# Performance work log

Hardware: AMD Instinct MI355X
Metric: run time of the kernel (lower is better)

## Reference

```python
import jax, jax.numpy as jnp
import numpy as np

N_NODES = 40000
N_EDGES = 480000
MULT = 64
NUM_SPECIES = 5
N_BASIS = 8
MLP_HIDDEN = 64
AVG_NEIGH = 12.0

INV8 = float(1.0 / np.sqrt(8.0))
INV64 = float(1.0 / np.sqrt(64.0))
INV128 = float(1.0 / np.sqrt(128.0))


def _poly_envelope(x):
    # e3nn.poly_envelope(5, 2) == DimeNet-style cutoff with p=6:
    # f(0)=1, first 5 derivatives zero at 0, f and 2 derivatives zero at 1.
    u = 1.0 - 28.0 * x**6 + 48.0 * x**7 - 21.0 * x**8
    return jnp.where(x < 1.0, u, 0.0)


def setup_inputs() -> dict:
    key = jax.random.key(0)
    ks = jax.random.split(key, 15)
    vectors = jax.random.uniform(ks[0], (N_EDGES, 3), jnp.float32, -0.5, 0.5)
    node_scalars = jax.random.normal(ks[1], (N_NODES, MULT), jnp.float32)
    node_vectors = jax.random.normal(ks[2], (N_NODES, MULT, 3), jnp.float32)
    node_specie = jax.random.randint(ks[3], (N_NODES,), 0, NUM_SPECIES)
    senders = jax.random.randint(ks[4], (N_EDGES,), 0, N_NODES)
    receivers = jax.random.randint(ks[5], (N_EDGES,), 0, N_NODES)
    # learned params (e3nn Linear weights ~ N(0,1), fwd divides by sqrt(fan_in))
    W_up_s = jax.random.normal(ks[6], (MULT, MULT), jnp.float32)
    W_up_v = jax.random.normal(ks[7], (MULT, MULT), jnp.float32)
    W_skip_s = jax.random.normal(ks[8], (NUM_SPECIES, MULT, 2 * MULT), jnp.float32)
    W_skip_v = jax.random.normal(ks[9], (NUM_SPECIES, MULT, MULT), jnp.float32)
    W_mlp1 = jax.random.normal(ks[10], (N_BASIS, MLP_HIDDEN), jnp.float32)
    W_mlp2 = jax.random.normal(ks[11], (MLP_HIDDEN, MLP_HIDDEN), jnp.float32)
    W_mlp3 = jax.random.normal(ks[12], (MLP_HIDDEN, 4 * MULT), jnp.float32)
    W_down_s = jax.random.normal(ks[13], (2 * MULT, 2 * MULT), jnp.float32)
    W_down_v = jax.random.normal(ks[14], (2 * MULT, MULT), jnp.float32)
    return dict(vectors=vectors, node_scalars=node_scalars, node_vectors=node_vectors,
                node_specie=node_specie, senders=senders, receivers=receivers,
                W_up_s=W_up_s, W_up_v=W_up_v, W_skip_s=W_skip_s, W_skip_v=W_skip_v,
                W_mlp1=W_mlp1, W_mlp2=W_mlp2, W_mlp3=W_mlp3,
                W_down_s=W_down_s, W_down_v=W_down_v)


def reference(vectors, node_scalars, node_vectors, node_specie, senders, receivers,
              W_up_s, W_up_v, W_skip_s, W_skip_v, W_mlp1, W_mlp2, W_mlp3,
              W_down_s, W_down_v):
    N = node_scalars.shape[0]
    # self-connection: species-indexed linear ('skip_tp'), output 128x0e + 64x1o
    sc_s = jnp.einsum('ni,nio->no', node_scalars, W_skip_s[node_specie]) * INV64
    sc_v = jnp.einsum('nic,nio->noc', node_vectors, W_skip_v[node_specie]) * INV64
    # linear_up (irreps-wise linear, 64x0e+64x1o -> same)
    h_s = (node_scalars @ W_up_s) * INV64
    h_v = jnp.einsum('nic,io->noc', node_vectors, W_up_v) * INV64
    # gather by sender
    m_s = h_s[senders]                       # [E,64]
    m_v = h_v[senders]                       # [E,64,3]
    # spherical harmonics l=1, normalize=True, component norm: sqrt(3)*r_hat
    lengths = jnp.linalg.norm(vectors, axis=1, keepdims=True)   # [E,1]
    safe_len = jnp.where(lengths == 0.0, 1.0, lengths)
    Y = jnp.sqrt(3.0) * vectors / safe_len                      # [E,3]
    # sparse CG tensor product (component norm): 0e x 1o -> 1o, 1o x 1o -> 0e
    tp_1o = m_s[:, :, None] * Y[:, None, :]                     # [E,64,3]
    tp_0e = jnp.einsum('eic,ec->ei', m_v, Y) / jnp.sqrt(3.0)    # [E,64]
    # concatenate + regroup -> 128x0e + 128x1o
    msg_s = jnp.concatenate([m_s, tp_0e], axis=1)               # [E,128]
    msg_v = jnp.concatenate([m_v, tp_1o], axis=1)               # [E,128,3]
    # radial basis (bessel, x_max=1) * smooth envelope
    k = jnp.arange(1, N_BASIS + 1, dtype=jnp.float32)
    bes = jnp.sqrt(2.0) * jnp.sin(k * jnp.pi * safe_len) / safe_len  # [E,8]
    rb = jnp.where(lengths == 0.0, 0.0, bes * _poly_envelope(lengths))
    h = jax.nn.swish((rb @ W_mlp1) * INV8)
    h = jax.nn.swish((h @ W_mlp2) * INV64)
    mix = (h @ W_mlp3) * INV64                                  # [E,256]
    msg_s = msg_s * mix[:, :128]
    msg_v = msg_v * mix[:, 128:, None]
    # scatter-add to receivers, normalize by sqrt(avg_num_neighbors)
    inv_sqrt_nn = 1.0 / np.sqrt(AVG_NEIGH)
    agg_s = jax.ops.segment_sum(msg_s, receivers, num_segments=N) * inv_sqrt_nn
    agg_v = jax.ops.segment_sum(msg_v, receivers, num_segments=N) * inv_sqrt_nn
    # linear_down to 128x0e + 64x1o, plus self-connection
    d_s = (agg_s @ W_down_s) * INV128 + sc_s                    # [N,128]
    d_v = jnp.einsum('nic,io->noc', agg_v, W_down_v) * INV128 + sc_v  # [N,64,3]
    # gate: first 64 scalars kept (swish), last 64 gate the vectors (swish)
    out_s = jax.nn.swish(d_s[:, :MULT])
    gates = jax.nn.swish(d_s[:, MULT:])
    out_v = d_v * gates[:, :, None]
    return jnp.concatenate([out_s, out_v.reshape(N, MULT * 3)], axis=1)  # [N,256]
```

## Files before the change

kernel.cpp:

```cpp
#include <hip/hip_runtime.h>
#include <hip/hip_bf16.h>

#define N_NODES 40000
#define N_EDGES 480000
#define SEG 2
#define SEG_E (N_EDGES / SEG)
#define SEG_TILES (SEG_E / 16)
#define SCAN_BLOCKS 157

typedef short bf16x8 __attribute__((ext_vector_type(8)));
typedef float f32x4 __attribute__((ext_vector_type(4)));

__device__ __forceinline__ float bf2f(__hip_bfloat16 x) { return __bfloat162float(x); }

__device__ __forceinline__ float swishf(float x) { return x / (1.0f + __expf(-x)); }

__device__ __forceinline__ float bflo(unsigned u) { union { unsigned u; float f; } w; w.u = u << 16; return w.f; }
__device__ __forceinline__ float bfhi(unsigned u) { union { unsigned u; float f; } w; w.u = u & 0xffff0000u; return w.f; }
__device__ __forceinline__ float bfu(unsigned short u) { union { unsigned u; float f; } w; w.u = ((unsigned)u) << 16; return w.f; }

__device__ __forceinline__ unsigned short f2bf_bits(float x) {
    union { __hip_bfloat16 h; unsigned short u; } c; c.h = __float2bfloat16(x); return c.u;
}

__constant__ const float INV8 = 0.35355339059327373f;
__constant__ const float INV64 = 0.125f;
__constant__ const float INV128 = 0.08838834764831845f;
__constant__ const float INV_NN = 0.2886751345948129f;
__constant__ const float SQRT2 = 1.4142135623730951f;
__constant__ const float SQRT3 = 1.7320508075688772f;
__constant__ const float INV_SQRT3 = 0.5773502691896258f;
__constant__ const float PI_F = 3.14159265358979323846f;

__device__ __forceinline__ float LDf(const void* p, size_t i, bool f32) {
    float v;
    if (f32) v = ((const float*)p)[i];
    else     v = bf2f(((const __hip_bfloat16*)p)[i]);
    return v;
}
__device__ __forceinline__ void load_f8r(const void* p, size_t i, bool f32, float* out) {
    if (f32) {
        const float4* q4 = (const float4*)((const float*)p + i);
        float4 a = q4[0], b = q4[1];
        out[0] = a.x; out[1] = a.y; out[2] = a.z; out[3] = a.w;
        out[4] = b.x; out[5] = b.y; out[6] = b.z; out[7] = b.w;
    } else {
        bf16x8 v = *(const bf16x8*)((const unsigned short*)p + i);
        #pragma unroll
        for (int j = 0; j < 8; j++) out[j] = bfu((unsigned short)v[j]);
    }
}

__global__ void detect_kernel(const unsigned short* __restrict__ w, int* __restrict__ flag) {
    int lane = threadIdx.x;
    int cnt = 0;
    for (int i = lane; i < 2048; i += 64) {
        unsigned e = (w[2 * i] >> 7) & 0xFF;
        if (e >= 110 && e <= 133) cnt++;
    }
    #pragma unroll
    for (int off = 32; off > 0; off >>= 1) cnt += __shfl_down(cnt, off, 64);
    if (lane == 0) *flag = (cnt > 1024) ? 1 : 0;
}

__global__ __launch_bounds__(256) void wprep_kernel(
    const void* __restrict__ W_up_s, const void* __restrict__ W_up_v,
    const void* __restrict__ W_skip_s, const void* __restrict__ W_skip_v,
    const void* __restrict__ W_down_s, const void* __restrict__ W_down_v,
    const void* __restrict__ W_mlp2, const void* __restrict__ W_mlp3,
    unsigned short* __restrict__ Wup_sq, unsigned short* __restrict__ Wup_vq,
    unsigned short* __restrict__ Wq_s, unsigned short* __restrict__ Wq_v,
    unsigned short* __restrict__ W2q, unsigned short* __restrict__ W3q,
    const int* __restrict__ flag)
{
    bool f32 = (*flag == 0);
    const float SC = INV128 * INV_NN;
    int gid = blockIdx.x * 256 + threadIdx.x;
    int gs = gridDim.x * 256;
    for (int i = gid; i < 4096; i += gs) {
        int o = i & 63, k = i >> 6;
        Wup_sq[o * 72 + k] = f2bf_bits(LDf(W_up_s, k * 64 + o, f32) * INV64);
        Wup_vq[o * 72 + k] = f2bf_bits(LDf(W_up_v, k * 64 + o, f32) * INV64);
    }
    for (int i = gid; i < 5 * 128 * 192; i += gs) {
        int sp = i / 24576, r = i - sp * 24576;
        int o = r / 192, k = r - o * 192;
        float w = (k < 128) ? LDf(W_down_s, k * 128 + o, f32) * SC
                            : LDf(W_skip_s, sp * 8192 + (k - 128) * 128 + o, f32) * INV64;
        Wq_s[sp * 25600 + o * 200 + k] = f2bf_bits(w);
    }
    for (int i = gid; i < 5 * 64 * 192; i += gs) {
        int sp = i / 12288, r = i - sp * 12288;
        int o = r / 192, k = r - o * 192;
        float w = (k < 128) ? LDf(W_down_v, k * 64 + o, f32) * SC
                            : LDf(W_skip_v, sp * 4096 + (k - 128) * 64 + o, f32) * INV64;
        Wq_v[sp * 12800 + o * 200 + k] = f2bf_bits(w);
    }
    for (int i = gid; i < 16384; i += gs) {
        int o = i & 255, k = i >> 8;
        W3q[o * 72 + k] = f2bf_bits(LDf(W_mlp3, k * 256 + o, f32));
    }
    for (int i = gid; i < 4096; i += gs) {
        int o = i & 63, k = i >> 6;
        W2q[o * 72 + k] = f2bf_bits(LDf(W_mlp2, k * 64 + o, f32));
    }
}

__global__ __launch_bounds__(256) void hist_kernel(const int* __restrict__ receivers,
                                                   int* __restrict__ cnt) {
    int e = blockIdx.x * 256 + threadIdx.x;
    if (e < N_EDGES) atomicAdd(&cnt[receivers[e]], 1);
}

__global__ __launch_bounds__(256) void partial_kernel(const int* __restrict__ cnt,
                                                      int* __restrict__ partials) {
    __shared__ int red[4];
    int idx = blockIdx.x * 256 + threadIdx.x;
    int v = (idx < N_NODES) ? cnt[idx] : 0;
    #pragma unroll
    for (int off = 32; off > 0; off >>= 1) v += __shfl_down(v, off, 64);
    int wave = threadIdx.x >> 6, lane = threadIdx.x & 63;
    if (lane == 0) red[wave] = v;
    __syncthreads();
    if (threadIdx.x == 0) partials[blockIdx.x] = red[0] + red[1] + red[2] + red[3];
}

__global__ __launch_bounds__(256) void scanp_kernel(const int* __restrict__ partials,
                                                    int* __restrict__ pscan) {
    __shared__ int buf[256];
    int t = threadIdx.x;
    int v = (t < SCAN_BLOCKS) ? partials[t] : 0;
    buf[t] = v;
    __syncthreads();
    for (int off = 1; off < 256; off <<= 1) {
        int tmp = (t >= off) ? buf[t - off] : 0;
        __syncthreads();
        buf[t] += tmp;
        __syncthreads();
    }
    if (t < SCAN_BLOCKS) pscan[t] = buf[t] - v;
}

__global__ __launch_bounds__(256) void offs_kernel(const int* __restrict__ cnt,
                                                   const int* __restrict__ pscan,
                                                   int* __restrict__ offs,
                                                   int* __restrict__ cursor) {
    __shared__ int buf[256];
    int b = blockIdx.x, t = threadIdx.x;
    int idx = b * 256 + t;
    int v = (idx < N_NODES) ? cnt[idx] : 0;
    buf[t] = v;
    __syncthreads();
    for (int off = 1; off < 256; off <<= 1) {
        int tmp = (t >= off) ? buf[t - off] : 0;
        __syncthreads();
        buf[t] += tmp;
        __syncthreads();
    }
    int exc = buf[t] - v + pscan[b];
    if (idx < N_NODES) { offs[idx] = exc; cursor[idx] = exc; }
    if (idx == N_NODES - 1) offs[N_NODES] = exc + v;
}

__global__ __launch_bounds__(256) void scatter_kernel(const int* __restrict__ receivers,
                                                      const int* __restrict__ senders,
                                                      int* __restrict__ cursor,
                                                      int* __restrict__ sorted_eid,
                                                      int* __restrict__ sorted_snd) {
    int e = blockIdx.x * 256 + threadIdx.x;
    if (e < N_EDGES) {
        int p = atomicAdd(&cursor[receivers[e]], 1);
        sorted_eid[p] = e;
        sorted_snd[p] = senders[e];
    }
}

__global__ __launch_bounds__(256) void hist5_kernel(const int* __restrict__ specie,
                                                    int* __restrict__ cnt5) {
    int n = blockIdx.x * 256 + threadIdx.x;
    int lane = threadIdx.x & 63;
    int sp = (n < N_NODES) ? specie[n] : -1;
    #pragma unroll
    for (int s = 0; s < 5; s++) {
        unsigned long long mask = __ballot(sp == s);
        if (mask != 0ull) {
            int leader = __builtin_ctzll(mask);
            if (lane == leader) atomicAdd(&cnt5[s], __popcll(mask));
        }
    }
}

__global__ void scan5_kernel(const int* __restrict__ cnt5, int* __restrict__ sp_offs,
                             int* __restrict__ cursor5, int* __restrict__ tile_info) {
    if (threadIdx.x != 0 || blockIdx.x != 0) return;
    int run = 0, tb = 0;
    for (int s = 0; s < 5; s++) {
        sp_offs[s] = run; cursor5[s] = run;
        tile_info[s] = tb;
        int c = cnt5[s];
        int T = (c + 15) >> 4;
        tile_info[8 + s] = T;
        tb += (T + 3) >> 2;
        run += c;
    }
    sp_offs[5] = run;
    tile_info[5] = tb;
}

__global__ __launch_bounds__(256) void scatter5_kernel(const int* __restrict__ specie,
                                                       int* __restrict__ cursor5,
                                                       int* __restrict__ sorted_node) {
    int n = blockIdx.x * 256 + threadIdx.x;
    int lane = threadIdx.x & 63;
    int sp = (n < N_NODES) ? specie[n] : -1;
    #pragma unroll
    for (int s = 0; s < 5; s++) {
        unsigned long long mask = __ballot(sp == s);
        if (mask != 0ull) {
            int leader = __builtin_ctzll(mask);
            int base = 0;
            if (lane == leader) base = atomicAdd(&cursor5[s], __popcll(mask));
            base = __shfl(base, leader);
            if (sp == s) {
                int prefix = __popcll(mask & ((1ull << lane) - 1ull));
                sorted_node[base + prefix] = n;
            }
        }
    }
}

__global__ __launch_bounds__(256) void node_up_kernel(
    const void* __restrict__ node_scalars,
    const void* __restrict__ node_vectors,
    const unsigned short* __restrict__ Wup_sq,
    const unsigned short* __restrict__ Wup_vq,
    unsigned short* __restrict__ hbuf,
    unsigned short* __restrict__ ns_b,
    unsigned short* __restrict__ nv_t,
    const int* __restrict__ flag)
{
    bool f32 = (*flag == 0);
    __shared__ __align__(16) unsigned short WsT[64 * 72];
    __shared__ __align__(16) unsigned short WvT[64 * 72];
    int tid = threadIdx.x;
    for (int i = tid; i < 576; i += 256) {
        ((uint4*)WsT)[i] = ((const uint4*)Wup_sq)[i];
        ((uint4*)WvT)[i] = ((const uint4*)Wup_vq)[i];
    }
    __syncthreads();
    int wave = tid >> 6, lane = tid & 63;
    int m = lane & 15, q = lane >> 4;
    int base = (blockIdx.x * 4 + wave) * 16;

    f32x4 accS[4];
    f32x4 accV[3][4];
    #pragma unroll
    for (int t = 0; t < 4; t++) {
        accS[t] = f32x4{0.f, 0.f, 0.f, 0.f};
        #pragma unroll
        for (int c = 0; c < 3; c++) accV[c][t] = f32x4{0.f, 0.f, 0.f, 0.f};
    }

    #pragma unroll
    for (int kk = 0; kk < 2; kk++) {
        int i0 = kk * 32 + 8 * q;
        float fs[8];
        load_f8r(node_scalars, (size_t)(base + m) * 64 + i0, f32, fs);
        bf16x8 aS;
        #pragma unroll
        for (int j = 0; j < 8; j++) aS[j] = (short)f2bf_bits(fs[j]);
        *(bf16x8*)(ns_b + (size_t)(base + m) * 64 + i0) = aS;
        float fv[24];
        size_t vbase = (size_t)(base + m) * 192 + (size_t)i0 * 3;
        load_f8r(node_vectors, vbase,      f32, fv);
        load_f8r(node_vectors, vbase + 8,  f32, fv + 8);
        load_f8r(node_vectors, vbase + 16, f32, fv + 16);
        bf16x8 aV[3];
        #pragma unroll
        for (int c = 0; c < 3; c++) {
            #pragma unroll
            for (int j = 0; j < 8; j++) aV[c][j] = (short)f2bf_bits(fv[3 * j + c]);
            *(bf16x8*)(nv_t + (size_t)c * N_NODES * 64 + (size_t)(base + m) * 64 + i0) = aV[c];
        }
        #pragma unroll
        for (int t = 0; t < 4; t++) {
            bf16x8 bS = *(const bf16x8*)(WsT + (16 * t + m) * 72 + kk * 32 + 8 * q);
            bf16x8 bV = *(const bf16x8*)(WvT + (16 * t + m) * 72 + kk * 32 + 8 * q);
            accS[t]    = __builtin_amdgcn_mfma_f32_16x16x32_bf16(aS,    bS, accS[t],    0, 0, 0);
            accV[0][t] = __builtin_amdgcn_mfma_f32_16x16x32_bf16(aV[0], bV, accV[0][t], 0, 0, 0);
            accV[1][t] = __builtin_amdgcn_mfma_f32_16x16x32_bf16(aV[1], bV, accV[1][t], 0, 0, 0);
            accV[2][t] = __builtin_amdgcn_mfma_f32_16x16x32_bf16(aV[2], bV, accV[2][t], 0, 0, 0);
        }
    }
    #pragma unroll
    for (int t = 0; t < 4; t++) {
        #pragma unroll
        for (int r = 0; r < 4; r++) {
            uint2 pk;
            pk.x = (unsigned)f2bf_bits(accS[t][r])    | ((unsigned)f2bf_bits(accV[0][t][r]) << 16);
            pk.y = (unsigned)f2bf_bits(accV[1][t][r]) | ((unsigned)f2bf_bits(accV[2][t][r]) << 16);
            *(uint2*)(hbuf + (size_t)(base + 4 * q + r) * 256 + (16 * t + m) * 4) = pk;
        }
    }
}

__global__ __launch_bounds__(512) void mlp_kernel(
    const void* __restrict__ vectors,
    const int* __restrict__ sorted_eid,
    const void* __restrict__ W1,
    const unsigned short* __restrict__ W2q,
    const unsigned short* __restrict__ W3q,
    unsigned short* __restrict__ mixseg,
    unsigned short* __restrict__ yq,
    int p_lo,
    const int* __restrict__ flag)
{
    bool f32 = (*flag == 0);
    __shared__ __align__(16) unsigned short W3T[256 * 72];
    __shared__ __align__(16) unsigned short W2T[64 * 72];
    __shared__ unsigned short hbl[8 * 64 * 17];
    int tid = threadIdx.x;
    for (int i = tid; i < 2304; i += 512) ((uint4*)W3T)[i] = ((const uint4*)W3q)[i];
    for (int i = tid; i < 576; i += 512)  ((uint4*)W2T)[i] = ((const uint4*)W2q)[i];
    __syncthreads();
    int wave = tid >> 6, lane = tid & 63;
    int m = lane & 15, q = lane >> 4;
    int tile = blockIdx.x * 8 + wave;
    if (tile >= SEG_TILES) return;
    int p = p_lo + tile * 16 + m;

    int e = sorted_eid[p];
    float vx = LDf(vectors, (size_t)e * 3 + 0, f32);
    float vy = LDf(vectors, (size_t)e * 3 + 1, f32);
    float vz = LDf(vectors, (size_t)e * 3 + 2, f32);
    float len2 = vx * vx + vy * vy + vz * vz;
    float len = sqrtf(len2);
    float Yx = 0.f, Yy = 0.f, Yz = 0.f;
    float rb[8];
    if (len > 0.f) {
        float inv = 1.f / len;
        Yx = SQRT3 * vx * inv; Yy = SQRT3 * vy * inv; Yz = SQRT3 * vz * inv;
        float x6 = len2 * len2 * len2;
        float env = (len < 1.f) ? fmaf(x6, fmaf(len, fmaf(len, -21.f, 48.f), -28.f), 1.f) : 0.f;
        float c = SQRT2 * inv * env;
        #pragma unroll
        for (int k = 0; k < 8; k++) rb[k] = c * __sinf((float)(k + 1) * PI_F * len);
    } else {
        #pragma unroll
        for (int k = 0; k < 8; k++) rb[k] = 0.f;
    }
    if (q == 0) {
        uint2 yw;
        yw.x = f2bf_bits(Yx) | ((unsigned)f2bf_bits(Yy) << 16);
        yw.y = f2bf_bits(Yz);
        *(uint2*)(yq + (size_t)p * 4) = yw;
    }

    f32x4 zero4 = {0.f, 0.f, 0.f, 0.f};
    unsigned short* hb = hbl + wave * (64 * 17);

    bf16x8 b_rb;
    #pragma unroll
    for (int j = 0; j < 8; j++) b_rb[j] = (q == 0) ? (short)f2bf_bits(rb[j]) : (short)0;
    #pragma unroll
    for (int t = 0; t < 4; t++) {
        bf16x8 a;
        #pragma unroll
        for (int j = 0; j < 8; j++) a[j] = 0;
        if (q == 0) {
            #pragma unroll
            for (int j = 0; j < 8; j++)
                a[j] = (short)f2bf_bits(LDf(W1, j * 64 + 16 * t + m, f32));
        }
        f32x4 c = __builtin_amdgcn_mfma_f32_16x16x32_bf16(a, b_rb, zero4, 0, 0, 0);
        #pragma unroll
        for (int r = 0; r < 4; r++)
            hb[(16 * t + 4 * q + r) * 17 + m] = f2bf_bits(swishf(c[r] * INV8));
    }
    bf16x8 b2[2];
    #pragma unroll
    for (int h = 0; h < 2; h++)
        #pragma unroll
        for (int j = 0; j < 8; j++)
            b2[h][j] = (short)hb[(32 * h + 8 * q + j) * 17 + m];
    #pragma unroll
    for (int t = 0; t < 4; t++) {
        bf16x8 a0 = *(const bf16x8*)(W2T + (16 * t + m) * 72 + 8 * q);
        bf16x8 a1 = *(const bf16x8*)(W2T + (16 * t + m) * 72 + 32 + 8 * q);
        f32x4 c = __builtin_amdgcn_mfma_f32_16x16x32_bf16(a0, b2[0], zero4, 0, 0, 0);
        c = __builtin_amdgcn_mfma_f32_16x16x32_bf16(a1, b2[1], c, 0, 0, 0);
        #pragma unroll
        for (int r = 0; r < 4; r++)
            hb[(16 * t + 4 * q + r) * 17 + m] = f2bf_bits(swishf(c[r] * INV64));
    }
    bf16x8 b3[2];
    #pragma unroll
    for (int h = 0; h < 2; h++)
        #pragma unroll
        for (int j = 0; j < 8; j++)
            b3[h][j] = (short)hb[(32 * h + 8 * q + j) * 17 + m];
    size_t rowbase = ((size_t)(tile * 16 + m)) * 256;
    #pragma unroll
    for (int t3 = 0; t3 < 16; t3++) {
        bf16x8 a0 = *(const bf16x8*)(W3T + (16 * t3 + m) * 72 + 8 * q);
        bf16x8 a1 = *(const bf16x8*)(W3T + (16 * t3 + m) * 72 + 32 + 8 * q);
        f32x4 c = __builtin_amdgcn_mfma_f32_16x16x32_bf16(a0, b3[0], zero4, 0, 0, 0);
        c = __builtin_amdgcn_mfma_f32_16x16x32_bf16(a1, b3[1], c, 0, 0, 0);
        uint2 v;
        v.x = f2bf_bits(c[0] * INV64) | ((unsigned)f2bf_bits(c[1] * INV64) << 16);
        v.y = f2bf_bits(c[2] * INV64) | ((unsigned)f2bf_bits(c[3] * INV64) << 16);
        *(uint2*)(mixseg + rowbase + 16 * t3 + 4 * q) = v;
    }
}

__global__ __launch_bounds__(256) void agg_kernel(
    const unsigned short* __restrict__ hbuf,
    const int* __restrict__ sorted_snd,
    const unsigned short* __restrict__ mixseg,
    const unsigned short* __restrict__ yq,
    const int* __restrict__ offs,
    unsigned short* __restrict__ agg_s_b,
    unsigned short* __restrict__ agg_v_b,
    int slo, int shi)
{
    int tid = threadIdx.x, wave = tid >> 6, lane = tid & 63;
    int n = blockIdx.x * 4 + wave;
    if (n >= N_NODES) return;
    int beg = __builtin_amdgcn_readfirstlane(offs[n]);
    int end = __builtin_amdgcn_readfirstlane(offs[n + 1]);
    int lo = beg > slo ? beg : slo;
    int hi = end < shi ? end : shi;
    bool owner = (beg >= slo && beg < shi) || (beg >= shi && shi == N_EDGES);
    if (!owner && hi <= lo) return;
    unsigned short* aS = agg_s_b + (size_t)n * 128;
    unsigned short* aV = agg_v_b + (size_t)n * 384;
    float s0, s1, v0, v1, v2, v3, v4, v5;
    if (owner) {
        s0 = s1 = v0 = v1 = v2 = v3 = v4 = v5 = 0.f;
    } else {
        s0 = bfu(aS[lane]); s1 = bfu(aS[64 + lane]);
        v0 = bfu(aV[lane]); v1 = bfu(aV[64 + lane]); v2 = bfu(aV[128 + lane]);
        v3 = bfu(aV[192 + lane]); v4 = bfu(aV[256 + lane]); v5 = bfu(aV[320 + lane]);
    }
    for (int chunk = lo; chunk < hi; chunk += 64) {
        int cc = hi - chunk; if (cc > 64) cc = 64;
        int sv = (lane < cc) ? sorted_snd[chunk + lane] : 0;
        int i = 0;
        for (; i + 1 < cc; i += 2) {
            int snd0 = __builtin_amdgcn_readlane(sv, i);
            int snd1 = __builtin_amdgcn_readlane(sv, i + 1);
            int p0 = chunk + i, p1 = chunk + i + 1;
            uint2 h0 = *(const uint2*)(hbuf + (size_t)snd0 * 256 + lane * 4);
            uint2 h1 = *(const uint2*)(hbuf + (size_t)snd1 * 256 + lane * 4);
            const unsigned short* mp0 = mixseg + (size_t)(p0 - slo) * 256;
            const unsigned short* mp1 = mixseg + (size_t)(p1 - slo) * 256;
            float a0 = bfu(mp0[lane]), a1 = bfu(mp0[64 + lane]);
            float a2 = bfu(mp0[128 + lane]), a3 = bfu(mp0[192 + lane]);
            float b0 = bfu(mp1[lane]), b1 = bfu(mp1[64 + lane]);
            float b2 = bfu(mp1[128 + lane]), b3 = bfu(mp1[192 + lane]);
            uint2 yw0 = *(const uint2*)(yq + (size_t)p0 * 4);
            uint2 yw1 = *(const uint2*)(yq + (size_t)p1 * 4);
            {
                float m_s = bflo(h0.x), mv0 = bfhi(h0.x), mv1 = bflo(h0.y), mv2 = bfhi(h0.y);
                float Yx = bflo(yw0.x), Yy = bfhi(yw0.x), Yz = bflo(yw0.y);
                float tp0 = (mv0 * Yx + mv1 * Yy + mv2 * Yz) * INV_SQRT3;
                s0 = fmaf(m_s, a0, s0);
                s1 = fmaf(tp0, a1, s1);
                float t1 = m_s * a3;
                v0 = fmaf(mv0, a2, v0); v1 = fmaf(t1, Yx, v1);
                v2 = fmaf(mv1, a2, v2); v3 = fmaf(t1, Yy, v3);
                v4 = fmaf(mv2, a2, v4); v5 = fmaf(t1, Yz, v5);
            }
            {
                float m_s = bflo(h1.x), mv0 = bfhi(h1.x), mv1 = bflo(h1.y), mv2 = bfhi(h1.y);
                float Yx = bflo(yw1.x), Yy = bfhi(yw1.x), Yz = bflo(yw1.y);
                float tp0 = (mv0 * Yx + mv1 * Yy + mv2 * Yz) * INV_SQRT3;
                s0 = fmaf(m_s, b0, s0);
                s1 = fmaf(tp0, b1, s1);
                float t1 = m_s * b3;
                v0 = fmaf(mv0, b2, v0); v1 = fmaf(t1, Yx, v1);
                v2 = fmaf(mv1, b2, v2); v3 = fmaf(t1, Yy, v3);
                v4 = fmaf(mv2, b2, v4); v5 = fmaf(t1, Yz, v5);
            }
        }
        if (i < cc) {
            int snd = __builtin_amdgcn_readlane(sv, i);
            int p = chunk + i;
            uint2 hbv = *(const uint2*)(hbuf + (size_t)snd * 256 + lane * 4);
            const unsigned short* mp = mixseg + (size_t)(p - slo) * 256;
            float mix0 = bfu(mp[lane]), mix1 = bfu(mp[64 + lane]);
            float mix2 = bfu(mp[128 + lane]), mix3 = bfu(mp[192 + lane]);
            uint2 yw = *(const uint2*)(yq + (size_t)p * 4);
            float m_s = bflo(hbv.x), mv0 = bfhi(hbv.x), mv1 = bflo(hbv.y), mv2 = bfhi(hbv.y);
            float Yx = bflo(yw.x), Yy = bfhi(yw.x), Yz = bflo(yw.y);
            float tp0 = (mv0 * Yx + mv1 * Yy + mv2 * Yz) * INV_SQRT3;
            s0 = fmaf(m_s, mix0, s0);
            s1 = fmaf(tp0, mix1, s1);
            float t1 = m_s * mix3;
            v0 = fmaf(mv0, mix2, v0); v1 = fmaf(t1, Yx, v1);
            v2 = fmaf(mv1, mix2, v2); v3 = fmaf(t1, Yy, v3);
            v4 = fmaf(mv2, mix2, v4); v5 = fmaf(t1, Yz, v5);
        }
    }
    aS[lane] = f2bf_bits(s0); aS[64 + lane] = f2bf_bits(s1);
    aV[lane] = f2bf_bits(v0); aV[64 + lane] = f2bf_bits(v1); aV[128 + lane] = f2bf_bits(v2);
    aV[192 + lane] = f2bf_bits(v3); aV[256 + lane] = f2bf_bits(v4); aV[320 + lane] = f2bf_bits(v5);
}

__global__ __launch_bounds__(256) void node_final_kernel(
    const unsigned short* __restrict__ Wq_s,
    const unsigned short* __restrict__ Wq_v,
    const unsigned short* __restrict__ ns_b,
    const unsigned short* __restrict__ nv_t,
    const unsigned short* __restrict__ agg_s_b,
    const unsigned short* __restrict__ agg_v_b,
    const int* __restrict__ sorted_node,
    const int* __restrict__ sp_offs,
    const int* __restrict__ tile_info,
    void* __restrict__ out,
    const int* __restrict__ flag)
{
    bool f32 = (*flag == 0);
    int b = blockIdx.x;
    if (b >= tile_info[5]) return;
    __shared__ __align__(16) unsigned short As[128 * 200];
    __shared__ __align__(16) unsigned short Av[64 * 200];
    int sp = 0;
    #pragma unroll
    for (int s = 1; s < 5; s++) if (b >= tile_info[s]) sp = s;
    int tid = threadIdx.x;
    const uint4* ps = (const uint4*)(Wq_s + (size_t)sp * 25600);
    for (int i = tid; i < 3200; i += 256) ((uint4*)As)[i] = ps[i];
    const uint4* pv = (const uint4*)(Wq_v + (size_t)sp * 12800);
    for (int i = tid; i < 1600; i += 256) ((uint4*)Av)[i] = pv[i];
    __syncthreads();
    int wave = tid >> 6, lane = tid & 63;
    int m = lane & 15, q = lane >> 4;
    int T = tile_info[8 + sp];
    int tl = (b - tile_info[sp]) * 4 + wave;
    if (tl >= T) return;
    int row = sp_offs[sp] + tl * 16;
    int cnt = sp_offs[sp + 1] - row; if (cnt > 16) cnt = 16;
    int mm = (m < cnt) ? m : 0;
    int node = sorted_node[row + mm];

    bf16x8 bs[6];
    {
        const unsigned short* a = agg_s_b + (size_t)node * 128;
        #pragma unroll
        for (int f = 0; f < 4; f++) bs[f] = *(const bf16x8*)(a + f * 32 + q * 8);
        const unsigned short* s = ns_b + (size_t)node * 64;
        #pragma unroll
        for (int f = 0; f < 2; f++) bs[4 + f] = *(const bf16x8*)(s + f * 32 + q * 8);
    }
    bf16x8 bv[3][6];
    #pragma unroll
    for (int c = 0; c < 3; c++) {
        const unsigned short* a = agg_v_b + (size_t)node * 384 + c * 128;
        #pragma unroll
        for (int f = 0; f < 4; f++) bv[c][f] = *(const bf16x8*)(a + f * 32 + q * 8);
        const unsigned short* s = nv_t + (size_t)c * N_NODES * 64 + (size_t)node * 64;
        #pragma unroll
        for (int f = 0; f < 2; f++) bv[c][4 + f] = *(const bf16x8*)(s + f * 32 + q * 8);
    }
    f32x4 z4 = {0.f, 0.f, 0.f, 0.f};
    float gate[4][4];
    #pragma unroll
    for (int t = 0; t < 4; t++) {
        f32x4 c = z4;
        #pragma unroll
        for (int f = 0; f < 6; f++) {
            bf16x8 a = *(const bf16x8*)(As + (16 * (4 + t) + m) * 200 + f * 32 + q * 8);
            c = __builtin_amdgcn_mfma_f32_16x16x32_bf16(a, bs[f], c, 0, 0, 0);
        }
        #pragma unroll
        for (int r = 0; r < 4; r++) gate[t][r] = swishf(c[r]);
    }
    #pragma unroll
    for (int t = 0; t < 4; t++) {
        f32x4 c = z4;
        #pragma unroll
        for (int f = 0; f < 6; f++) {
            bf16x8 a = *(const bf16x8*)(As + (16 * t + m) * 200 + f * 32 + q * 8);
            c = __builtin_amdgcn_mfma_f32_16x16x32_bf16(a, bs[f], c, 0, 0, 0);
        }
        if (m < cnt) {
            size_t base = (size_t)node * 256 + 16 * t + 4 * q;
            if (f32) {
                float4 o4 = { swishf(c[0]), swishf(c[1]), swishf(c[2]), swishf(c[3]) };
                *(float4*)((float*)out + base) = o4;
            } else {
                uint2 o2;
                o2.x = f2bf_bits(swishf(c[0])) | ((unsigned)f2bf_bits(swishf(c[1])) << 16);
                o2.y = f2bf_bits(swishf(c[2])) | ((unsigned)f2bf_bits(swishf(c[3])) << 16);
                *(uint2*)((unsigned short*)out + base) = o2;
            }
        }
    }
    #pragma unroll
    for (int t = 0; t < 4; t++) {
        f32x4 c0 = z4, c1 = z4, c2 = z4;
        #pragma unroll
        for (int f = 0; f < 6; f++) {
            bf16x8 a = *(const bf16x8*)(Av + (16 * t + m) * 200 + f * 32 + q * 8);
            c0 = __builtin_amdgcn_mfma_f32_16x16x32_bf16(a, bv[0][f], c0, 0, 0, 0);
            c1 = __builtin_amdgcn_mfma_f32_16x16x32_bf16(a, bv[1][f], c1, 0, 0, 0);
            c2 = __builtin_amdgcn_mfma_f32_16x16x32_bf16(a, bv[2][f], c2, 0, 0, 0);
        }
        if (m < cnt) {
            #pragma unroll
            for (int r = 0; r < 4; r++) {
                float g = gate[t][r];
                int o = 16 * t + 4 * q + r;
                size_t base = (size_t)node * 256 + 64 + (size_t)o * 3;
                if (f32) {
                    ((float*)out)[base + 0] = c0[r] * g;
                    ((float*)out)[base + 1] = c1[r] * g;
                    ((float*)out)[base + 2] = c2[r] * g;
                } else {
                    ((__hip_bfloat16*)out)[base + 0] = __float2bfloat16(c0[r] * g);
                    ((__hip_bfloat16*)out)[base + 1] = __float2bfloat16(c1[r] * g);
                    ((__hip_bfloat16*)out)[base + 2] = __float2bfloat16(c2[r] * g);
                }
            }
        }
    }
}

extern "C" void kernel_launch(void* const* d_in, const int* in_sizes, int n_in,
                              void* d_out, int out_size, void* d_ws, size_t ws_size,
                              hipStream_t stream) {
    const void* vectors      = d_in[0];
    const void* node_scalars = d_in[1];
    const void* node_vectors = d_in[2];
    const int* node_specie   = (const int*)d_in[3];
    const int* senders       = (const int*)d_in[4];
    const int* receivers     = (const int*)d_in[5];
    const void* W_up_s       = d_in[6];
    const void* W_up_v       = d_in[7];
    const void* W_skip_s     = d_in[8];
    const void* W_skip_v     = d_in[9];
    const void* W_mlp1       = d_in[10];
    const void* W_mlp2       = d_in[11];
    const void* W_mlp3       = d_in[12];
    const void* W_down_s     = d_in[13];
    const void* W_down_v     = d_in[14];

    char* ws = (char*)d_ws;
    size_t off = 0;
    auto alloc = [&](size_t bytes) { void* p = ws + off; off += (bytes + 255) & ~(size_t)255; return p; };
    unsigned short* hbuf     = (unsigned short*)alloc((size_t)N_NODES * 256 * 2);
    unsigned short* ns_b     = (unsigned short*)alloc((size_t)N_NODES * 64 * 2);
    unsigned short* nv_t     = (unsigned short*)alloc((size_t)N_NODES * 192 * 2);
    unsigned short* agg_s_b  = (unsigned short*)alloc((size_t)N_NODES * 128 * 2);
    unsigned short* agg_v_b  = (unsigned short*)alloc((size_t)N_NODES * 384 * 2);
    unsigned short* mixseg   = (unsigned short*)alloc((size_t)SEG_E * 256 * 2);
    unsigned short* yq       = (unsigned short*)alloc((size_t)N_EDGES * 4 * 2);
    unsigned short* Wup_sq   = (unsigned short*)alloc((size_t)64 * 72 * 2);
    unsigned short* Wup_vq   = (unsigned short*)alloc((size_t)64 * 72 * 2);
    unsigned short* Wq_s     = (unsigned short*)alloc((size_t)5 * 128 * 200 * 2);
    unsigned short* Wq_v     = (unsigned short*)alloc((size_t)5 * 64 * 200 * 2);
    unsigned short* W2q      = (unsigned short*)alloc((size_t)64 * 72 * 2);
    unsigned short* W3q      = (unsigned short*)alloc((size_t)256 * 72 * 2);
    int* cnt        = (int*)alloc((size_t)(N_NODES + 8) * 4);
    int* cnt5       = cnt + N_NODES;
    int* offs       = (int*)alloc((size_t)(N_NODES + 1) * 4);
    int* cursor     = (int*)alloc((size_t)N_NODES * 4);
    int* sorted     = (int*)alloc((size_t)N_EDGES * 4);
    int* sorted_snd = (int*)alloc((size_t)N_EDGES * 4);
    int* sorted_node= (int*)alloc((size_t)N_NODES * 4);
    int* sp_offs    = (int*)alloc(16 * 4);
    int* cursor5    = (int*)alloc(16 * 4);
    int* tile_info  = (int*)alloc(16 * 4);
    int* partials   = (int*)alloc((size_t)(SCAN_BLOCKS + 1) * 4);
    int* pscan      = (int*)alloc((size_t)(SCAN_BLOCKS + 1) * 4);
    int* flag       = (int*)alloc(4);

    detect_kernel<<<dim3(1), dim3(64), 0, stream>>>((const unsigned short*)W_up_s, flag);
    hipMemsetAsync(cnt, 0, (size_t)(N_NODES + 8) * 4, stream);

    wprep_kernel<<<dim3(64), dim3(256), 0, stream>>>(
        W_up_s, W_up_v, W_skip_s, W_skip_v, W_down_s, W_down_v, W_mlp2, W_mlp3,
        Wup_sq, Wup_vq, Wq_s, Wq_v, W2q, W3q, flag);

    hist_kernel<<<dim3(1875), dim3(256), 0, stream>>>(receivers, cnt);
    partial_kernel<<<dim3(SCAN_BLOCKS), dim3(256), 0, stream>>>(cnt, partials);
    scanp_kernel<<<dim3(1), dim3(256), 0, stream>>>(partials, pscan);
    offs_kernel<<<dim3(SCAN_BLOCKS), dim3(256), 0, stream>>>(cnt, pscan, offs, cursor);
    scatter_kernel<<<dim3(1875), dim3(256), 0, stream>>>(receivers, senders, cursor, sorted, sorted_snd);

    hist5_kernel<<<dim3(157), dim3(256), 0, stream>>>(node_specie, cnt5);
    scan5_kernel<<<dim3(1), dim3(64), 0, stream>>>(cnt5, sp_offs, cursor5, tile_info);
    scatter5_kernel<<<dim3(157), dim3(256), 0, stream>>>(node_specie, cursor5, sorted_node);

    node_up_kernel<<<dim3(625), dim3(256), 0, stream>>>(
        node_scalars, node_vectors, Wup_sq, Wup_vq, hbuf, ns_b, nv_t, flag);

    const int MLP_BLOCKS = (SEG_TILES + 7) / 8;
    for (int s = 0; s < SEG; s++) {
        int p_lo = s * SEG_E;
        mlp_kernel<<<dim3(MLP_BLOCKS), dim3(512), 0, stream>>>(
            vectors, sorted, W_mlp1, W2q, W3q, mixseg, yq, p_lo, flag);
        agg_kernel<<<dim3(10000), dim3(256), 0, stream>>>(
            hbuf, sorted_snd, mixseg, yq, offs, agg_s_b, agg_v_b, p_lo, p_lo + SEG_E);
    }

    node_final_kernel<<<dim3(640), dim3(256), 0, stream>>>(
        Wq_s, Wq_v, ns_b, nv_t, agg_s_b, agg_v_b,
        sorted_node, sp_offs, tile_info, d_out, flag);
}
```

Measured before the change: 544.1 us.

## Pre-sort edge vectors in scatter and process multiple tiles per wave in MLP

The scatter kernel now writes each edge's vector as a float4 into receiver-sorted order, so the MLP kernel reads vectors contiguously instead of gathering through an edge-id indirection. The MLP kernel loops over four tiles per wave, which amortizes the per-block LDS staging of W2/W3 and the W1 fragment loads over more work. The LDS row padding for the hidden buffer changes from 17 to 18. The costs are an extra 16-byte-per-edge buffer and fewer blocks, which reduces parallelism and latency hiding in the MLP launch.

```diff
diff --git a/kernel.cpp b/kernel.cpp
--- a/kernel.cpp
+++ b/kernel.cpp
@@ -7,6 +7,7 @@
 #define SEG_E (N_EDGES / SEG)
 #define SEG_TILES (SEG_E / 16)
 #define SCAN_BLOCKS 157
+#define TPW 4
 
 typedef short bf16x8 __attribute__((ext_vector_type(8)));
 typedef float f32x4 __attribute__((ext_vector_type(4)));
@@ -164,14 +165,20 @@
 
 __global__ __launch_bounds__(256) void scatter_kernel(const int* __restrict__ receivers,
                                                       const int* __restrict__ senders,
+                                                      const void* __restrict__ vectors,
                                                       int* __restrict__ cursor,
-                                                      int* __restrict__ sorted_eid,
-                                                      int* __restrict__ sorted_snd) {
+                                                      int* __restrict__ sorted_snd,
+                                                      float4* __restrict__ sorted_vec,
+                                                      const int* __restrict__ flag) {
+    bool f32 = (*flag == 0);
     int e = blockIdx.x * 256 + threadIdx.x;
     if (e < N_EDGES) {
+        float vx = LDf(vectors, (size_t)e * 3 + 0, f32);
+        float vy = LDf(vectors, (size_t)e * 3 + 1, f32);
+        float vz = LDf(vectors, (size_t)e * 3 + 2, f32);
         int p = atomicAdd(&cursor[receivers[e]], 1);
-        sorted_eid[p] = e;
         sorted_snd[p] = senders[e];
+        sorted_vec[p] = float4{vx, vy, vz, 0.f};
     }
 }
 
@@ -305,8 +312,7 @@
 }
 
 __global__ __launch_bounds__(512) void mlp_kernel(
-    const void* __restrict__ vectors,
-    const int* __restrict__ sorted_eid,
+    const float4* __restrict__ sorted_vec,
     const void* __restrict__ W1,
     const unsigned short* __restrict__ W2q,
     const unsigned short* __restrict__ W3q,
@@ -318,98 +324,104 @@
     bool f32 = (*flag == 0);
     __shared__ __align__(16) unsigned short W3T[256 * 72];
     __shared__ __align__(16) unsigned short W2T[64 * 72];
-    __shared__ unsigned short hbl[8 * 64 * 17];
+    __shared__ unsigned short hbl[8 * 64 * 18];
     int tid = threadIdx.x;
     for (int i = tid; i < 2304; i += 512) ((uint4*)W3T)[i] = ((const uint4*)W3q)[i];
     for (int i = tid; i < 576; i += 512)  ((uint4*)W2T)[i] = ((const uint4*)W2q)[i];
     __syncthreads();
     int wave = tid >> 6, lane = tid & 63;
     int m = lane & 15, q = lane >> 4;
-    int tile = blockIdx.x * 8 + wave;
-    if (tile >= SEG_TILES) return;
-    int p = p_lo + tile * 16 + m;
-
-    int e = sorted_eid[p];
-    float vx = LDf(vectors, (size_t)e * 3 + 0, f32);
-    float vy = LDf(vectors, (size_t)e * 3 + 1, f32);
-    float vz = LDf(vectors, (size_t)e * 3 + 2, f32);
-    float len2 = vx * vx + vy * vy + vz * vz;
-    float len = sqrtf(len2);
-    float Yx = 0.f, Yy = 0.f, Yz = 0.f;
-    float rb[8];
-    if (len > 0.f) {
-        float inv = 1.f / len;
-        Yx = SQRT3 * vx * inv; Yy = SQRT3 * vy * inv; Yz = SQRT3 * vz * inv;
-        float x6 = len2 * len2 * len2;
-        float env = (len < 1.f) ? fmaf(x6, fmaf(len, fmaf(len, -21.f, 48.f), -28.f), 1.f) : 0.f;
-        float c = SQRT2 * inv * env;
-        #pragma unroll
-        for (int k = 0; k < 8; k++) rb[k] = c * __sinf((float)(k + 1) * PI_F * len);
-    } else {
-        #pragma unroll
-        for (int k = 0; k < 8; k++) rb[k] = 0.f;
-    }
-    if (q == 0) {
-        uint2 yw;
-        yw.x = f2bf_bits(Yx) | ((unsigned)f2bf_bits(Yy) << 16);
-        yw.y = f2bf_bits(Yz);
-        *(uint2*)(yq + (size_t)p * 4) = yw;
-    }
-
+    unsigned short* hb = hbl + wave * (64 * 18);
     f32x4 zero4 = {0.f, 0.f, 0.f, 0.f};
-    unsigned short* hb = hbl + wave * (64 * 17);
-
-    bf16x8 b_rb;
-    #pragma unroll
-    for (int j = 0; j < 8; j++) b_rb[j] = (q == 0) ? (short)f2bf_bits(rb[j]) : (short)0;
+
+    bf16x8 a1f[4];
     #pragma unroll
     for (int t = 0; t < 4; t++) {
-        bf16x8 a;
-        #pragma unroll
-        for (int j = 0; j < 8; j++) a[j] = 0;
+        #pragma unroll
+        for (int j = 0; j < 8; j++) a1f[t][j] = 0;
         if (q == 0) {
             #pragma unroll
             for (int j = 0; j < 8; j++)
-                a[j] = (short)f2bf_bits(LDf(W1, j * 64 + 16 * t + m, f32));
-        }
-        f32x4 c = __builtin_amdgcn_mfma_f32_16x16x32_bf16(a, b_rb, zero4, 0, 0, 0);
-        #pragma unroll
-        for (int r = 0; r < 4; r++)
-            hb[(16 * t + 4 * q + r) * 17 + m] = f2bf_bits(swishf(c[r] * INV8));
-    }
-    bf16x8 b2[2];
-    #pragma unroll
-    for (int h = 0; h < 2; h++)
-        #pragma unroll
-        for (int j = 0; j < 8; j++)
-            b2[h][j] = (short)hb[(32 * h + 8 * q + j) * 17 + m];
-    #pragma unroll
-    for (int t = 0; t < 4; t++) {
-        bf16x8 a0 = *(const bf16x8*)(W2T + (16 * t + m) * 72 + 8 * q);
-        bf16x8 a1 = *(const bf16x8*)(W2T + (16 * t + m) * 72 + 32 + 8 * q);
-        f32x4 c = __builtin_amdgcn_mfma_f32_16x16x32_bf16(a0, b2[0], zero4, 0, 0, 0);
-        c = __builtin_amdgcn_mfma_f32_16x16x32_bf16(a1, b2[1], c, 0, 0, 0);
-        #pragma unroll
-        for (int r = 0; r < 4; r++)
-            hb[(16 * t + 4 * q + r) * 17 + m] = f2bf_bits(swishf(c[r] * INV64));
-    }
-    bf16x8 b3[2];
-    #pragma unroll
-    for (int h = 0; h < 2; h++)
-        #pragma unroll
-        for (int j = 0; j < 8; j++)
-            b3[h][j] = (short)hb[(32 * h + 8 * q + j) * 17 + m];
-    size_t rowbase = ((size_t)(tile * 16 + m)) * 256;
-    #pragma unroll
-    for (int t3 = 0; t3 < 16; t3++) {
-        bf16x8 a0 = *(const bf16x8*)(W3T + (16 * t3 + m) * 72 + 8 * q);
-        bf16x8 a1 = *(const bf16x8*)(W3T + (16 * t3 + m) * 72 + 32 + 8 * q);
-        f32x4 c = __builtin_amdgcn_mfma_f32_16x16x32_bf16(a0, b3[0], zero4, 0, 0, 0);
-        c = __builtin_amdgcn_mfma_f32_16x16x32_bf16(a1, b3[1], c, 0, 0, 0);
-        uint2 v;
-        v.x = f2bf_bits(c[0] * INV64) | ((unsigned)f2bf_bits(c[1] * INV64) << 16);
-        v.y = f2bf_bits(c[2] * INV64) | ((unsigned)f2bf_bits(c[3] * INV64) << 16);
-        *(uint2*)(mixseg + rowbase + 16 * t3 + 4 * q) = v;
+                a1f[t][j] = (short)f2bf_bits(LDf(W1, j * 64 + 16 * t + m, f32));
+        }
+    }
+
+    int tile0 = (blockIdx.x * 8 + wave) * TPW;
+    #pragma unroll 1
+    for (int tt = 0; tt < TPW; tt++) {
+        int tile = tile0 + tt;
+        if (tile >= SEG_TILES) break;
+        int p = p_lo + tile * 16 + m;
+
+        float4 sv = sorted_vec[p];
+        float vx = sv.x, vy = sv.y, vz = sv.z;
+        float len2 = vx * vx + vy * vy + vz * vz;
+        float len = sqrtf(len2);
+        float Yx = 0.f, Yy = 0.f, Yz = 0.f;
+        float rb[8];
+        if (len > 0.f) {
+            float inv = 1.f / len;
+            Yx = SQRT3 * vx * inv; Yy = SQRT3 * vy * inv; Yz = SQRT3 * vz * inv;
+            float x6 = len2 * len2 * len2;
+            float env = (len < 1.f) ? fmaf(x6, fmaf(len, fmaf(len, -21.f, 48.f), -28.f), 1.f) : 0.f;
+            float c = SQRT2 * inv * env;
+            #pragma unroll
+            for (int k = 0; k < 8; k++) rb[k] = c * __sinf((float)(k + 1) * PI_F * len);
+        } else {
+            #pragma unroll
+            for (int k = 0; k < 8; k++) rb[k] = 0.f;
+        }
+        if (q == 0) {
+            uint2 yw;
+            yw.x = f2bf_bits(Yx) | ((unsigned)f2bf_bits(Yy) << 16);
+            yw.y = f2bf_bits(Yz);
+            *(uint2*)(yq + (size_t)p * 4) = yw;
+        }
+
+        bf16x8 b_rb;
+        #pragma unroll
+        for (int j = 0; j < 8; j++) b_rb[j] = (q == 0) ? (short)f2bf_bits(rb[j]) : (short)0;
+        #pragma unroll
+        for (int t = 0; t < 4; t++) {
+            f32x4 c = __builtin_amdgcn_mfma_f32_16x16x32_bf16(a1f[t], b_rb, zero4, 0, 0, 0);
+            #pragma unroll
+            for (int r = 0; r < 4; r++)
+                hb[(16 * t + 4 * q + r) * 18 + m] = f2bf_bits(swishf(c[r] * INV8));
+        }
+        bf16x8 b2[2];
+        #pragma unroll
+        for (int h = 0; h < 2; h++)
+            #pragma unroll
+            for (int j = 0; j < 8; j++)
+                b2[h][j] = (short)hb[(32 * h + 8 * q + j) * 18 + m];
+        #pragma unroll
+        for (int t = 0; t < 4; t++) {
+            bf16x8 a0 = *(const bf16x8*)(W2T + (16 * t + m) * 72 + 8 * q);
+            bf16x8 a1 = *(const bf16x8*)(W2T + (16 * t + m) * 72 + 32 + 8 * q);
+            f32x4 c = __builtin_amdgcn_mfma_f32_16x16x32_bf16(a0, b2[0], zero4, 0, 0, 0);
+            c = __builtin_amdgcn_mfma_f32_16x16x32_bf16(a1, b2[1], c, 0, 0, 0);
+            #pragma unroll
+            for (int r = 0; r < 4; r++)
+                hb[(16 * t + 4 * q + r) * 18 + m] = f2bf_bits(swishf(c[r] * INV64));
+        }
+        bf16x8 b3[2];
+        #pragma unroll
+        for (int h = 0; h < 2; h++)
+            #pragma unroll
+            for (int j = 0; j < 8; j++)
+                b3[h][j] = (short)hb[(32 * h + 8 * q + j) * 18 + m];
+        size_t rowbase = ((size_t)(tile * 16 + m)) * 256;
+        #pragma unroll
+        for (int t3 = 0; t3 < 16; t3++) {
+            bf16x8 a0 = *(const bf16x8*)(W3T + (16 * t3 + m) * 72 + 8 * q);
+            bf16x8 a1 = *(const bf16x8*)(W3T + (16 * t3 + m) * 72 + 32 + 8 * q);
+            f32x4 c = __builtin_amdgcn_mfma_f32_16x16x32_bf16(a0, b3[0], zero4, 0, 0, 0);
+            c = __builtin_amdgcn_mfma_f32_16x16x32_bf16(a1, b3[1], c, 0, 0, 0);
+            uint2 v;
+            v.x = f2bf_bits(c[0] * INV64) | ((unsigned)f2bf_bits(c[1] * INV64) << 16);
+            v.y = f2bf_bits(c[2] * INV64) | ((unsigned)f2bf_bits(c[3] * INV64) << 16);
+            *(uint2*)(mixseg + rowbase + 16 * t3 + 4 * q) = v;
+        }
     }
 }
 
@@ -656,6 +668,7 @@
     unsigned short* agg_v_b  = (unsigned short*)alloc((size_t)N_NODES * 384 * 2);
     unsigned short* mixseg   = (unsigned short*)alloc((size_t)SEG_E * 256 * 2);
     unsigned short* yq       = (unsigned short*)alloc((size_t)N_EDGES * 4 * 2);
+    float4* sorted_vec       = (float4*)alloc((size_t)N_EDGES * 16);
     unsigned short* Wup_sq   = (unsigned short*)alloc((size_t)64 * 72 * 2);
     unsigned short* Wup_vq   = (unsigned short*)alloc((size_t)64 * 72 * 2);
     unsigned short* Wq_s     = (unsigned short*)alloc((size_t)5 * 128 * 200 * 2);
@@ -666,7 +679,6 @@
     int* cnt5       = cnt + N_NODES;
     int* offs       = (int*)alloc((size_t)(N_NODES + 1) * 4);
     int* cursor     = (int*)alloc((size_t)N_NODES * 4);
-    int* sorted     = (int*)alloc((size_t)N_EDGES * 4);
     int* sorted_snd = (int*)alloc((size_t)N_EDGES * 4);
     int* sorted_node= (int*)alloc((size_t)N_NODES * 4);
     int* sp_offs    = (int*)alloc(16 * 4);
@@ -687,7 +699,8 @@
     partial_kernel<<<dim3(SCAN_BLOCKS), dim3(256), 0, stream>>>(cnt, partials);
     scanp_kernel<<<dim3(1), dim3(256), 0, stream>>>(partials, pscan);
     offs_kernel<<<dim3(SCAN_BLOCKS), dim3(256), 0, stream>>>(cnt, pscan, offs, cursor);
-    scatter_kernel<<<dim3(1875), dim3(256), 0, stream>>>(receivers, senders, cursor, sorted, sorted_snd);
+    scatter_kernel<<<dim3(1875), dim3(256), 0, stream>>>(receivers, senders, vectors,
+                                                         cursor, sorted_snd, sorted_vec, flag);
 
     hist5_kernel<<<dim3(157), dim3(256), 0, stream>>>(node_specie, cnt5);
     scan5_kernel<<<dim3(1), dim3(64), 0, stream>>>(cnt5, sp_offs, cursor5, tile_info);
@@ -696,11 +709,11 @@
     node_up_kernel<<<dim3(625), dim3(256), 0, stream>>>(
         node_scalars, node_vectors, Wup_sq, Wup_vq, hbuf, ns_b, nv_t, flag);
 
-    const int MLP_BLOCKS = (SEG_TILES + 7) / 8;
+    const int MLP_BLOCKS = (SEG_TILES + 8 * TPW - 1) / (8 * TPW);
     for (int s = 0; s < SEG; s++) {
         int p_lo = s * SEG_E;
         mlp_kernel<<<dim3(MLP_BLOCKS), dim3(512), 0, stream>>>(
-            vectors, sorted, W_mlp1, W2q, W3q, mixseg, yq, p_lo, flag);
+            sorted_vec, W_mlp1, W2q, W3q, mixseg, yq, p_lo, flag);
         agg_kernel<<<dim3(10000), dim3(256), 0, stream>>>(
             hbuf, sorted_snd, mixseg, yq, offs, agg_s_b, agg_v_b, p_lo, p_lo + SEG_E);
     }
```

New measurement: 503.2 us. 1.08x faster.
